# Kernel optimization log

Measured on AMD Instinct MI355X. Metric: run time of the kernel, lower is better.

## Reference

```python
import jax, jax.numpy as jnp
import numpy as np

B, Q, K, D, H = 8, 1024, 1024, 1024, 16
HD = D // H
FFN = 4 * D


def layer_norm(x, w, b, eps=1e-5):
    mu = jnp.mean(x, axis=-1, keepdims=True)
    var = jnp.var(x, axis=-1, keepdims=True)
    return (x - mu) * jax.lax.rsqrt(var + eps) * w + b


def setup_inputs() -> dict:
    key = jax.random.key(0)
    ks = jax.random.split(key, 10)
    query = jax.random.normal(ks[0], (B, Q, D), dtype=jnp.float32)
    key_value = jax.random.normal(ks[1], (B, K, D), dtype=jnp.float32)
    kpm = jax.random.randint(ks[2], (B, K), 0, 2).astype(bool)
    kpm = kpm.at[:, 0].set(True)  # guarantee >=1 valid key per row
    s = 0.02
    return {
        "query": query,
        "key_value": key_value,
        "key_padding_mask": kpm,
        "ln_q_w": jnp.ones((D,), jnp.float32), "ln_q_b": jnp.zeros((D,), jnp.float32),
        "ln_kv_w": jnp.ones((D,), jnp.float32), "ln_kv_b": jnp.zeros((D,), jnp.float32),
        "ln_f_w": jnp.ones((D,), jnp.float32), "ln_f_b": jnp.zeros((D,), jnp.float32),
        "in_proj_w": jax.random.normal(ks[3], (3 * D, D), jnp.float32) * s,
        "in_proj_b": jnp.zeros((3 * D,), jnp.float32),
        "out_proj_w": jax.random.normal(ks[4], (D, D), jnp.float32) * s,
        "out_proj_b": jnp.zeros((D,), jnp.float32),
        "ffn_w1": jax.random.normal(ks[5], (FFN, D), jnp.float32) * s,
        "ffn_b1": jnp.zeros((FFN,), jnp.float32),
        "ffn_w2": jax.random.normal(ks[6], (D, FFN), jnp.float32) * s,
        "ffn_b2": jnp.zeros((D,), jnp.float32),
    }


def reference(query, key_value, key_padding_mask,
              ln_q_w, ln_q_b, ln_kv_w, ln_kv_b, ln_f_w, ln_f_b,
              in_proj_w, in_proj_b, out_proj_w, out_proj_b,
              ffn_w1, ffn_b1, ffn_w2, ffn_b2):
    q_norm = layer_norm(query, ln_q_w, ln_q_b)
    kv_norm = layer_norm(key_value, ln_kv_w, ln_kv_b)

    Wq, Wk, Wv = jnp.split(in_proj_w, 3, axis=0)
    bq, bk, bv = jnp.split(in_proj_b, 3, axis=0)
    q = (q_norm @ Wq.T + bq).reshape(B, Q, H, HD).transpose(0, 2, 1, 3)  # (B,H,Q,hd)
    k = (kv_norm @ Wk.T + bk).reshape(B, K, H, HD).transpose(0, 2, 1, 3)
    v = (kv_norm @ Wv.T + bv).reshape(B, K, H, HD).transpose(0, 2, 1, 3)

    scale = 1.0 / jnp.sqrt(jnp.float32(HD))
    scores = jnp.einsum('bhqd,bhkd->bhqk', q * scale, k)  # (B,H,Q,K)
    scores = jnp.where(key_padding_mask[:, None, None, :], scores, -jnp.inf)
    attn = jax.nn.softmax(scores, axis=-1)

    attn_out = jnp.einsum('bhqk,bhkd->bhqd', attn, v)
    attn_out = attn_out.transpose(0, 2, 1, 3).reshape(B, Q, D)
    attn_out = attn_out @ out_proj_w.T + out_proj_b

    x = query + attn_out
    h = layer_norm(x, ln_f_w, ln_f_b)
    h = jax.nn.gelu(h @ ffn_w1.T + ffn_b1, approximate=False)
    x = x + (h @ ffn_w2.T + ffn_b2)

    attn_weights = jnp.mean(attn, axis=1)  # average over heads -> (B,Q,K)
    return x, attn_weights
```

## Files before the change

kernel.cpp:

```cpp
#include <hip/hip_runtime.h>
#include <math.h>

typedef short  s16x8 __attribute__((ext_vector_type(8)));
typedef short  s16x4 __attribute__((ext_vector_type(4)));
typedef float  f32x4 __attribute__((ext_vector_type(4)));

#define DEV static __device__ __forceinline__
#define M0SHIFT 3.0f
#define LOG2E   1.44269504088896f
#define SCL2F   0.18033688011112f

#if __has_builtin(__builtin_amdgcn_exp2f)
#define EXP2F(x) __builtin_amdgcn_exp2f(x)
#else
#define EXP2F(x) exp2f(x)
#endif

DEV float b2f(unsigned short h) {
    unsigned int u = ((unsigned int)h) << 16;
    float f; __builtin_memcpy(&f, &u, 4); return f;
}
DEV unsigned short f2b(float f) {
    unsigned int u; __builtin_memcpy(&u, &f, 4);
    unsigned int r = (u + 0x7fffu + ((u >> 16) & 1u)) >> 16;
    return (unsigned short)r;
}
DEV unsigned fb(float x) { unsigned u; __builtin_memcpy(&u, &x, 4); return u; }
DEV s16x4 pack4(float a0, float a1, float a2, float a3) {
    unsigned lo = __builtin_amdgcn_perm(fb(a1), fb(a0), 0x07060302u);
    unsigned hi = __builtin_amdgcn_perm(fb(a3), fb(a2), 0x07060302u);
    unsigned long long p = ((unsigned long long)hi << 32) | lo;
    s16x4 r; __builtin_memcpy(&r, &p, 8); return r;
}

#define GLD16(gp, lp) __builtin_amdgcn_global_load_lds( \
    (const __attribute__((address_space(1))) unsigned int*)(const void*)(gp), \
    (__attribute__((address_space(3))) unsigned int*)(void*)(lp), 16, 0, 0)

#if __has_builtin(__builtin_amdgcn_mfma_f32_16x16x16_bf16)
#define MFMA16(a, b, c) __builtin_amdgcn_mfma_f32_16x16x16_bf16(a, b, c, 0, 0, 0)
#else
#define MFMA16(a, b, c) __builtin_amdgcn_mfma_f32_16x16x16bf16_1k(a, b, c, 0, 0, 0)
#endif

DEV float ldsel(const void* p, size_t i, bool f32) {
    return f32 ? ((const float*)p)[i] : b2f(((const unsigned short*)p)[i]);
}
DEV s16x8 ld8sel(const void* p, size_t eidx, bool f32) {
    if (f32) {
        const float* f = (const float*)p + eidx;
        f32x4 a = *(const f32x4*)f;
        f32x4 b = *(const f32x4*)(f + 4);
        s16x8 o;
        o[0]=(short)f2b(a[0]); o[1]=(short)f2b(a[1]); o[2]=(short)f2b(a[2]); o[3]=(short)f2b(a[3]);
        o[4]=(short)f2b(b[0]); o[5]=(short)f2b(b[1]); o[6]=(short)f2b(b[2]); o[7]=(short)f2b(b[3]);
        return o;
    }
    return *(const s16x8*)((const unsigned short*)p + eidx);
}

__global__ __launch_bounds__(256) void dtype_probe(
    const unsigned int* __restrict__ q, int* __restrict__ flag)
{
    int t = threadIdx.x;
    int hits = 0;
    for (int i = t; i < 2048; i += 256) {
        unsigned e0 = (q[i] >> 7) & 0xFFu;
        hits += (e0 >= 0x70u && e0 <= 0x87u) ? 1 : 0;
    }
#pragma unroll
    for (int m = 32; m >= 1; m >>= 1) hits += __shfl_xor(hits, m);
    __shared__ int sh[4];
    if ((t & 63) == 0) sh[t >> 6] = hits;
    __syncthreads();
    if (t == 0) *flag = (sh[0] + sh[1] + sh[2] + sh[3] > 1024) ? 0 : 1;
}

__global__ __launch_bounds__(1024) void mask_prep(
    const unsigned int* __restrict__ w, const unsigned char* __restrict__ bytes,
    float* __restrict__ mf)
{
    __shared__ int flag;
    const int t = threadIdx.x;
    if (t == 0) flag = 0;
    __syncthreads();
    unsigned int a = w[t], b = w[t + 1024];
    if (a > 1u || b > 1u) flag = 1;
    __syncthreads();
    const int f = flag;
    const float NEGINF = -__builtin_inff();
#pragma unroll
    for (int i = 0; i < 8; i++) {
        int c = t * 8 + i;
        int v = f ? (int)(bytes[c] != 0) : (int)(w[c] != 0);
        mf[c] = v ? (-M0SHIFT * LOG2E) : NEGINF;
    }
}

struct CvtArgs { const void* s[8]; };
__global__ __launch_bounds__(256) void cvt_w(
    const int* __restrict__ flagp, CvtArgs a, unsigned short* __restrict__ dst)
{
    const int f = *flagp;
    size_t e = ((size_t)blockIdx.x * 256 + threadIdx.x) * 8;
    if (e >= 12592128u) return;
    const size_t off[9] = {0u, 3145728u, 4194304u, 8388608u, 12582912u,
                           12585984u, 12587008u, 12591104u, 12592128u};
    int s = 0;
    while (e >= off[s + 1]) s++;
    *(s16x8*)&dst[e] = ld8sel(a.s[s], e - off[s], f == 1);
}

__global__ __launch_bounds__(256) void ln_k(
    const int* __restrict__ flagp, int xmode, int wmode,
    const void* __restrict__ x1p, const void* __restrict__ w1p, const void* __restrict__ b1p,
    unsigned short* __restrict__ y1p,
    const void* __restrict__ x2p, const void* __restrict__ w2p, const void* __restrict__ b2p,
    unsigned short* __restrict__ y2p)
{
    const int f = *flagp;
    const bool xf = (xmode == 2) ? (f == 1) : (xmode == 1);
    const bool wf = (wmode == 2) ? (f == 1) : (wmode == 1);
    int row = blockIdx.x;
    const void* x = x1p; const void* wgt = w1p; const void* bias = b1p;
    unsigned short* y = y1p;
    if (x2p && row >= 8192) {
        row -= 8192; x = x2p; wgt = w2p; bias = b2p; y = y2p;
    }
    const int t = threadIdx.x;
    const int w = t >> 6, lane = t & 63;
    float f0, f1, f2, f3;
    if (xf) {
        f32x4 v = *(const f32x4*)((const float*)x + (size_t)row * 1024 + t * 4);
        f0 = v[0]; f1 = v[1]; f2 = v[2]; f3 = v[3];
    } else {
        s16x4 v = *(const s16x4*)((const unsigned short*)x + (size_t)row * 1024 + t * 4);
        f0 = b2f((unsigned short)v[0]); f1 = b2f((unsigned short)v[1]);
        f2 = b2f((unsigned short)v[2]); f3 = b2f((unsigned short)v[3]);
    }
    __shared__ float red[4];
    float s = f0 + f1 + f2 + f3;
#pragma unroll
    for (int m = 32; m >= 1; m >>= 1) s += __shfl_xor(s, m);
    if (lane == 0) red[w] = s;
    __syncthreads();
    float mu = (red[0] + red[1] + red[2] + red[3]) * (1.0f / 1024.0f);
    float d0 = f0 - mu, d1 = f1 - mu, d2 = f2 - mu, d3 = f3 - mu;
    float q = d0 * d0 + d1 * d1 + d2 * d2 + d3 * d3;
#pragma unroll
    for (int m = 32; m >= 1; m >>= 1) q += __shfl_xor(q, m);
    __syncthreads();
    if (lane == 0) red[w] = q;
    __syncthreads();
    float var = (red[0] + red[1] + red[2] + red[3]) * (1.0f / 1024.0f);
    float rs = rsqrtf(var + 1e-5f);
    s16x4 vo;
    vo[0] = (short)f2b(d0 * rs * ldsel(wgt, t*4+0, wf) + ldsel(bias, t*4+0, wf));
    vo[1] = (short)f2b(d1 * rs * ldsel(wgt, t*4+1, wf) + ldsel(bias, t*4+1, wf));
    vo[2] = (short)f2b(d2 * rs * ldsel(wgt, t*4+2, wf) + ldsel(bias, t*4+2, wf));
    vo[3] = (short)f2b(d3 * rs * ldsel(wgt, t*4+3, wf) + ldsel(bias, t*4+3, wf));
    *(s16x4*)&y[(size_t)row * 1024 + t * 4] = vo;
}

__global__ __launch_bounds__(256) void gemm_bt(
    const int* __restrict__ flagp,
    const unsigned short* __restrict__ A,
    const void* __restrict__ W, size_t woff, int wmode,
    const void* __restrict__ bias, size_t boff, int bmode,
    const void* __restrict__ res, int rmode,
    void* __restrict__ C, int omode,
    int M, int N, int Kd, int ldw, int ldc, int act)
{
    const int f = *flagp;
    const bool wf = (wmode == 2) && (f == 1);
    __shared__ alignas(16) unsigned short As[128 * 32];
    __shared__ alignas(16) unsigned short Bs[128 * 32];
    const int t = threadIdx.x;
    const int m0 = blockIdx.y * 128, n0 = blockIdx.x * 128;
    const int w = t >> 6, lane = t & 63, quad = lane >> 4, l16 = lane & 15;
    const int wm = (w >> 1) * 64, wn = (w & 1) * 64;
    const f32x4 zero = {0.f, 0.f, 0.f, 0.f};
    f32x4 acc[4][4];
#pragma unroll
    for (int i = 0; i < 4; i++)
#pragma unroll
        for (int j = 0; j < 4; j++) acc[i][j] = zero;
    const int r0 = t >> 2, c0 = (t & 3) * 8;
    unsigned short* AsW = As + (size_t)w * 512;
    unsigned short* BsW = Bs + (size_t)w * 512;
    const unsigned short* W16 = (const unsigned short*)W + woff;
    const float*          W32 = (const float*)W + woff;

    for (int kt = 0; kt < Kd; kt += 32) {
        GLD16(&A[(size_t)(m0 + r0) * Kd + kt + c0],      AsW);
        GLD16(&A[(size_t)(m0 + r0 + 64) * Kd + kt + c0], AsW + 2048);
        if (wf) {
            *(s16x8*)&Bs[r0 * 32 + c0]        = ld8sel(W32, (size_t)(n0 + r0) * ldw + kt + c0, true);
            *(s16x8*)&Bs[(r0 + 64) * 32 + c0] = ld8sel(W32, (size_t)(n0 + r0 + 64) * ldw + kt + c0, true);
        } else {
            GLD16(&W16[(size_t)(n0 + r0) * ldw + kt + c0],      BsW);
            GLD16(&W16[(size_t)(n0 + r0 + 64) * ldw + kt + c0], BsW + 2048);
        }
        __syncthreads();
        s16x8 af[4], bfr[4];
#pragma unroll
        for (int i = 0; i < 4; i++) {
            af[i]  = *(const s16x8*)&As[(wm + i * 16 + l16) * 32 + quad * 8];
            bfr[i] = *(const s16x8*)&Bs[(wn + i * 16 + l16) * 32 + quad * 8];
        }
#pragma unroll
        for (int mi = 0; mi < 4; mi++)
#pragma unroll
            for (int ni = 0; ni < 4; ni++)
                acc[mi][ni] = __builtin_amdgcn_mfma_f32_16x16x32_bf16(af[mi], bfr[ni], acc[mi][ni], 0, 0, 0);
        __syncthreads();
    }
    const bool bf = (bmode == 2) && (f == 1);
    const bool rf = (rmode == 2) || (rmode == 3 && f == 1);
    const bool of = (omode == 1) || (omode == 2 && f == 1);
#pragma unroll
    for (int mi = 0; mi < 4; mi++)
#pragma unroll
        for (int ni = 0; ni < 4; ni++)
#pragma unroll
            for (int r = 0; r < 4; r++) {
                int gr = m0 + wm + mi * 16 + quad * 4 + r;
                int gc = n0 + wn + ni * 16 + l16;
                float v = acc[mi][ni][r];
                if (bmode >= 0) v += ldsel(bias, boff + gc, bf);
                if (act) v = 0.5f * v * (1.f + erff(v * 0.70710678118f));
                if (rmode) v += ldsel(res, (size_t)gr * ldc + gc, rf);
                size_t ci = (size_t)gr * ldc + gc;
                if (of) ((float*)C)[ci] = v;
                else ((unsigned short*)C)[ci] = f2b(v);
            }
}

__global__ __launch_bounds__(512, 2) void gemm8(
    const unsigned short* __restrict__ A,
    const unsigned short* __restrict__ W, size_t woff,
    const unsigned short* __restrict__ bias, size_t boff,
    unsigned short* __restrict__ C,
    int Kd, int ldc, int act)
{
    __shared__ alignas(16) unsigned short lds[65536];
    const unsigned short* Wp = W + woff;
    const int t = threadIdx.x;
    const int w = t >> 6, lane = t & 63, quad = lane >> 4, l16 = lane & 15;
    const int wr = w >> 2, wcn = w & 3;

    const int gx = (int)gridDim.x;
    const int nwg = gx * (int)gridDim.y;
    const int lid = (int)blockIdx.y * gx + (int)blockIdx.x;
    const int swz = (lid & 7) * (nwg >> 3) + (lid >> 3);
    const int m0 = (swz / gx) * 256, n0 = (swz % gx) * 256;

    const int hrow = w * 16 + (lane >> 3);
    const int scol = ((lane & 7) ^ ((lane & 32) ? 2 : 0)) * 8;
    const int NT = Kd >> 6;

    const int swq = (l16 & 4) ? 16 : 0;
    const int ck0 = (quad * 8) ^ swq;
    const int ck1 = (32 + quad * 8) ^ swq;

    const f32x4 zero = {0.f, 0.f, 0.f, 0.f};
    f32x4 acc[8][4];
#pragma unroll
    for (int i = 0; i < 8; i++)
#pragma unroll
        for (int j = 0; j < 4; j++) acc[i][j] = zero;
    s16x8 aF[4][2], bLo[2][2], bHi[2][2];

#define SA8(bb,h,tt,g) GLD16(&A[(size_t)(m0 + (h)*128 + hrow + (g)*8) * Kd + (size_t)(tt)*64 + scol], \
                             &lds[(bb)*32768 + (h)*8192 + (w*16 + (g)*8)*64])
#define SB8(bb,h,tt,g) GLD16(&Wp[(size_t)(n0 + (h)*128 + hrow + (g)*8) * Kd + (size_t)(tt)*64 + scol], \
                             &lds[(bb)*32768 + 16384 + (h)*8192 + (w*16 + (g)*8)*64])
#define LDA8(bb,q) { _Pragma("unroll") for (int i_ = 0; i_ < 4; i_++) { \
        const int ar_ = (q)*128 + wr*64 + i_*16 + l16; \
        aF[i_][0] = *(const s16x8*)&lds[(bb)*32768 + ar_*64 + ck0]; \
        aF[i_][1] = *(const s16x8*)&lds[(bb)*32768 + ar_*64 + ck1]; } }
#define LDB8(bb,dst,q) { _Pragma("unroll") for (int j_ = 0; j_ < 2; j_++) { \
        const int br_ = (q)*128 + wcn*32 + j_*16 + l16; \
        dst[j_][0] = *(const s16x8*)&lds[(bb)*32768 + 16384 + br_*64 + ck0]; \
        dst[j_][1] = *(const s16x8*)&lds[(bb)*32768 + 16384 + br_*64 + ck1]; } }
#define MM8(mq,nq,bsrc) { __builtin_amdgcn_s_setprio(1); \
        _Pragma("unroll") for (int i_ = 0; i_ < 4; i_++) \
        _Pragma("unroll") for (int j_ = 0; j_ < 2; j_++) { \
            acc[(mq)*4+i_][(nq)*2+j_] = __builtin_amdgcn_mfma_f32_16x16x32_bf16(aF[i_][0], bsrc[j_][0], acc[(mq)*4+i_][(nq)*2+j_], 0, 0, 0); \
            acc[(mq)*4+i_][(nq)*2+j_] = __builtin_amdgcn_mfma_f32_16x16x32_bf16(aF[i_][1], bsrc[j_][1], acc[(mq)*4+i_][(nq)*2+j_], 0, 0, 0); } \
        __builtin_amdgcn_s_setprio(0); }
#define BAR8() __builtin_amdgcn_s_barrier()
#define VMW8(n) asm volatile("s_waitcnt vmcnt(" #n ")" ::: "memory")

    SA8(0, 0, 0, 0); SA8(0, 0, 0, 1);
    SB8(0, 0, 0, 0); SB8(0, 0, 0, 1);
    SB8(0, 1, 0, 0); SB8(0, 1, 0, 1);
    SA8(0, 1, 0, 0); SA8(0, 1, 0, 1);
    VMW8(4); BAR8();

    for (int tt = 0; tt < NT - 1; tt++) {
        const int bb = tt & 1, nb = bb ^ 1;
        SA8(nb, 0, tt + 1, 0); SA8(nb, 0, tt + 1, 1);
        LDA8(bb, 0); LDB8(bb, bLo, 0);
        MM8(0, 0, bLo);
        VMW8(4); BAR8();
        SB8(nb, 0, tt + 1, 0); SB8(nb, 0, tt + 1, 1);
        LDB8(bb, bHi, 1);
        MM8(0, 1, bHi);
        VMW8(4); BAR8();
        SB8(nb, 1, tt + 1, 0); SB8(nb, 1, tt + 1, 1);
        LDA8(bb, 1);
        MM8(1, 1, bHi);
        BAR8();
        SA8(nb, 1, tt + 1, 0); SA8(nb, 1, tt + 1, 1);
        MM8(1, 0, bLo);
        VMW8(4); BAR8();
    }
    {
        const int bb = (NT - 1) & 1;
        LDA8(bb, 0); LDB8(bb, bLo, 0); MM8(0, 0, bLo); VMW8(2); BAR8();
        LDB8(bb, bHi, 1);              MM8(0, 1, bHi); VMW8(0); BAR8();
        LDA8(bb, 1);                   MM8(1, 1, bHi);
        MM8(1, 0, bLo);
    }

#pragma unroll
    for (int nq = 0; nq < 2; nq++)
#pragma unroll
    for (int j = 0; j < 2; j++) {
        const int gc = n0 + nq * 128 + wcn * 32 + j * 16 + l16;
        const float bv = b2f(bias[boff + gc]);
#pragma unroll
        for (int mq = 0; mq < 2; mq++)
#pragma unroll
        for (int i = 0; i < 4; i++)
#pragma unroll
        for (int r = 0; r < 4; r++) {
            const int gr = m0 + mq * 128 + wr * 64 + i * 16 + quad * 4 + r;
            float v = acc[mq * 4 + i][nq * 2 + j][r] + bv;
            if (act) v = 0.5f * v * (1.f + erff(v * 0.70710678118f));
            C[(size_t)gr * ldc + gc] = f2b(v);
        }
    }
#undef SA8
#undef SB8
#undef LDA8
#undef LDB8
#undef MM8
#undef BAR8
#undef VMW8
}

__global__ __launch_bounds__(256) void repack_kv(
    const unsigned short* __restrict__ kvp,
    unsigned short* __restrict__ kf, unsigned short* __restrict__ vf)
{
    const bool isv = blockIdx.x >= 4096;
    int t = (blockIdx.x - (isv ? 4096 : 0)) * 256 + threadIdx.x;
    int lane = t & 63;
    int quad = lane >> 4, l16 = lane & 15;
    if (!isv) {
        int half = (t >> 6) & 1, tile = (t >> 7) & 63;
        int h = (t >> 13) & 15, b = t >> 17;
        s16x8 v = *(const s16x8*)&kvp[(size_t)(b * 1024 + tile * 16 + l16) * 2048
                                      + h * 64 + half * 32 + quad * 8];
        *(s16x8*)&kf[(size_t)t * 8] = v;
    } else {
        int dt = (t >> 6) & 3, kt5 = (t >> 8) & 31;
        int h = (t >> 13) & 15, b = t >> 17;
        int d = dt * 16 + l16;
        s16x8 o;
#pragma unroll
        for (int j = 0; j < 8; j++) {
            int k = kt5 * 32 + ((j < 4) ? (quad * 4 + j) : (16 + quad * 4 + j - 4));
            o[j] = (short)kvp[(size_t)(b * 1024 + k) * 2048 + 1024 + h * 64 + d];
        }
        *(s16x8*)&vf[(size_t)t * 8] = o;
    }
}

__global__ __launch_bounds__(256, 4) void flash_attn(
    const unsigned short* __restrict__ qp, const unsigned short* __restrict__ kf,
    const unsigned short* __restrict__ vf, const float* __restrict__ maskf,
    unsigned short* __restrict__ ao, float* __restrict__ ml)
{
    const int bh = blockIdx.x;
    const int b = bh >> 4, h = bh & 15;
    const int t = threadIdx.x, w = t >> 6, lane = t & 63, quad = lane >> 4, l16 = lane & 15;
    const int q0 = (blockIdx.y * 4 + w) * 32;
    const f32x4 zero = {0.f, 0.f, 0.f, 0.f};

    const unsigned short* kfb = kf + (size_t)bh * 65536;
    const unsigned short* vfb = vf + (size_t)bh * 65536;

    const size_t qbA = (size_t)(b * 1024 + q0 + l16) * 1024 + h * 64 + quad * 8;
    const size_t qbB = qbA + (size_t)16 * 1024;
    s16x8 qa0 = *(const s16x8*)&qp[qbA], qa1 = *(const s16x8*)&qp[qbA + 32];
    s16x8 qb0 = *(const s16x8*)&qp[qbB], qb1 = *(const s16x8*)&qp[qbB + 32];

    f32x4 OA[4], OB[4];
#pragma unroll
    for (int dt = 0; dt < 4; dt++) { OA[dt] = zero; OB[dt] = zero; }
    float lsA = 0.f, lsB = 0.f;

    for (int kt = 0; kt < 1024; kt += 32) {
        const int tile2 = (kt >> 4) * 2;
        s16x8 k00 = *(const s16x8*)&kfb[(size_t)(tile2 + 0) * 512 + lane * 8];
        s16x8 k01 = *(const s16x8*)&kfb[(size_t)(tile2 + 1) * 512 + lane * 8];
        s16x8 k10 = *(const s16x8*)&kfb[(size_t)(tile2 + 2) * 512 + lane * 8];
        s16x8 k11 = *(const s16x8*)&kfb[(size_t)(tile2 + 3) * 512 + lane * 8];
        const size_t vrow = (size_t)(kt >> 5) * 4;
        s16x8 vv[4];
#pragma unroll
        for (int dt = 0; dt < 4; dt++)
            vv[dt] = *(const s16x8*)&vfb[(vrow + dt) * 512 + lane * 8];

        f32x4 SA0 = __builtin_amdgcn_mfma_f32_16x16x32_bf16(k00, qa0, zero, 0, 0, 0);
        SA0 = __builtin_amdgcn_mfma_f32_16x16x32_bf16(k01, qa1, SA0, 0, 0, 0);
        f32x4 SA1 = __builtin_amdgcn_mfma_f32_16x16x32_bf16(k10, qa0, zero, 0, 0, 0);
        SA1 = __builtin_amdgcn_mfma_f32_16x16x32_bf16(k11, qa1, SA1, 0, 0, 0);
        f32x4 SB0 = __builtin_amdgcn_mfma_f32_16x16x32_bf16(k00, qb0, zero, 0, 0, 0);
        SB0 = __builtin_amdgcn_mfma_f32_16x16x32_bf16(k01, qb1, SB0, 0, 0, 0);
        f32x4 SB1 = __builtin_amdgcn_mfma_f32_16x16x32_bf16(k10, qb0, zero, 0, 0, 0);
        SB1 = __builtin_amdgcn_mfma_f32_16x16x32_bf16(k11, qb1, SB1, 0, 0, 0);

        f32x4 mk0 = *(const f32x4*)&maskf[b * 1024 + kt + quad * 4];
        f32x4 mk1 = *(const f32x4*)&maskf[b * 1024 + kt + 16 + quad * 4];
        float xA0[4], xA1[4], xB0[4], xB1[4];
#pragma unroll
        for (int r = 0; r < 4; r++) {
            xA0[r] = EXP2F(SA0[r] * SCL2F + mk0[r]);
            xA1[r] = EXP2F(SA1[r] * SCL2F + mk1[r]);
            xB0[r] = EXP2F(SB0[r] * SCL2F + mk0[r]);
            xB1[r] = EXP2F(SB1[r] * SCL2F + mk1[r]);
        }
        float rsA = (xA0[0] + xA0[1]) + (xA0[2] + xA0[3])
                  + (xA1[0] + xA1[1]) + (xA1[2] + xA1[3]);
        float rsB = (xB0[0] + xB0[1]) + (xB0[2] + xB0[3])
                  + (xB1[0] + xB1[1]) + (xB1[2] + xB1[3]);
        rsA += __shfl_xor(rsA, 16);  rsA += __shfl_xor(rsA, 32);
        rsB += __shfl_xor(rsB, 16);  rsB += __shfl_xor(rsB, 32);
        lsA += rsA;  lsB += rsB;

        s16x4 pA0 = pack4(xA0[0], xA0[1], xA0[2], xA0[3]);
        s16x4 pA1 = pack4(xA1[0], xA1[1], xA1[2], xA1[3]);
        s16x4 pB0 = pack4(xB0[0], xB0[1], xB0[2], xB0[3]);
        s16x4 pB1 = pack4(xB1[0], xB1[1], xB1[2], xB1[3]);
#pragma unroll
        for (int dt = 0; dt < 4; dt++) {
            s16x4 v0 = {vv[dt][0], vv[dt][1], vv[dt][2], vv[dt][3]};
            s16x4 v1 = {vv[dt][4], vv[dt][5], vv[dt][6], vv[dt][7]};
            OA[dt] = MFMA16(pA0, v0, OA[dt]);
            OA[dt] = MFMA16(pA1, v1, OA[dt]);
            OB[dt] = MFMA16(pB0, v0, OB[dt]);
            OB[dt] = MFMA16(pB1, v1, OB[dt]);
        }
    }
    float liA = (lsA > 0.f) ? 1.f / lsA : 0.f;
    float liB = (lsB > 0.f) ? 1.f / lsB : 0.f;
    float libA[4], libB[4];
#pragma unroll
    for (int r = 0; r < 4; r++) {
        libA[r] = __shfl(liA, quad * 4 + r);
        libB[r] = __shfl(liB, quad * 4 + r);
    }
#pragma unroll
    for (int dt = 0; dt < 4; dt++)
#pragma unroll
        for (int r = 0; r < 4; r++) {
            int qrA = q0 + quad * 4 + r;
            ao[(size_t)(b * 1024 + qrA) * 1024 + h * 64 + dt * 16 + l16] = f2b(OA[dt][r] * libA[r]);
            ao[(size_t)(b * 1024 + qrA + 16) * 1024 + h * 64 + dt * 16 + l16] = f2b(OB[dt][r] * libB[r]);
        }
    if (lane < 16) {
        size_t ix = ((size_t)(b * 16 + h) * 1024 + q0 + l16) * 2;
        ml[ix] = M0SHIFT;      ml[ix + 1] = lsA;
        ml[ix + 32] = M0SHIFT; ml[ix + 33] = lsB;
    }
}

__global__ __launch_bounds__(256) void attn_mean_k(
    const int* __restrict__ flagp,
    const unsigned short* __restrict__ qp, const unsigned short* __restrict__ kf,
    const float* __restrict__ maskf, const float* __restrict__ ml,
    void* __restrict__ dout)
{
    const bool of = (*flagp == 1);
    const size_t SHIFT = (size_t)8 * 1024 * 1024;
    const int b = blockIdx.x, q0 = blockIdx.y * 16;
    const int t = threadIdx.x, w = t >> 6, lane = t & 63, quad = lane >> 4, l16 = lane & 15;
    const int kbase = w * 256;
    const f32x4 zero = {0.f, 0.f, 0.f, 0.f};
    f32x4 acc[16];
#pragma unroll
    for (int i = 0; i < 16; i++) acc[i] = zero;
    float mka[16];
#pragma unroll
    for (int i = 0; i < 16; i++)
        mka[i] = maskf[b * 1024 + kbase + i * 16 + l16];
    for (int h = 0; h < 16; h++) {
        const size_t qb = (size_t)(b * 1024 + q0 + l16) * 1024 + h * 64 + quad * 8;
        s16x8 a0 = *(const s16x8*)&qp[qb];
        s16x8 a1 = *(const s16x8*)&qp[qb + 32];
        float cexp[4], lirow[4];
#pragma unroll
        for (int r = 0; r < 4; r++) {
            size_t ix = ((size_t)(b * 16 + h) * 1024 + q0 + quad * 4 + r) * 2;
            float lv = ml[ix + 1];
            cexp[r] = (M0SHIFT - ml[ix]) * LOG2E;
            lirow[r] = (lv > 0.f) ? 1.f / lv : 0.f;
        }
        const unsigned short* kfb = kf + ((size_t)(b * 16 + h) * 128 + (kbase >> 4) * 2) * 512;
#pragma unroll
        for (int i = 0; i < 16; i++) {
            s16x8 b0 = *(const s16x8*)&kfb[(size_t)(i * 2 + 0) * 512 + lane * 8];
            s16x8 b1 = *(const s16x8*)&kfb[(size_t)(i * 2 + 1) * 512 + lane * 8];
            f32x4 S = __builtin_amdgcn_mfma_f32_16x16x32_bf16(a0, b0, zero, 0, 0, 0);
            S = __builtin_amdgcn_mfma_f32_16x16x32_bf16(a1, b1, S, 0, 0, 0);
#pragma unroll
            for (int r = 0; r < 4; r++)
                acc[i][r] += EXP2F(S[r] * SCL2F + mka[i] + cexp[r]) * lirow[r];
        }
    }
#pragma unroll
    for (int i = 0; i < 16; i++)
#pragma unroll
        for (int r = 0; r < 4; r++) {
            int qrow = q0 + quad * 4 + r;
            size_t oi = SHIFT + (size_t)(b * 1024 + qrow) * 1024 + kbase + i * 16 + l16;
            float v = acc[i][r] * 0.0625f;
            if (of) ((float*)dout)[oi] = v;
            else ((unsigned short*)dout)[oi] = f2b(v);
        }
}

extern "C" void kernel_launch(void* const* d_in, const int* in_sizes, int n_in,
                              void* d_out, int out_size, void* d_ws, size_t ws_size,
                              hipStream_t stream) {
    const void* query = d_in[0];
    const void* keyv  = d_in[1];
    const void* maskr = d_in[2];
    const void* lqw = d_in[3];  const void* lqb = d_in[4];
    const void* lkw = d_in[5];  const void* lkb = d_in[6];
    const void* lfw = d_in[7];  const void* lfb = d_in[8];
    const void* ipw = d_in[9];  const void* ipb = d_in[10];
    const void* opw = d_in[11]; const void* opb = d_in[12];
    const void* w1  = d_in[13]; const void* b1  = d_in[14];
    const void* w2  = d_in[15]; const void* b2  = d_in[16];

    char* ws = (char*)d_ws;
    const size_t MB = 1024 * 1024;
    unsigned short* qn  = (unsigned short*)(ws + 0 * MB);
    unsigned short* kvn = (unsigned short*)(ws + 16 * MB);
    unsigned short* qpj = (unsigned short*)(ws + 32 * MB);
    unsigned short* kvp = (unsigned short*)(ws + 48 * MB);
    unsigned short* kfr = (unsigned short*)(ws + 80 * MB);
    unsigned short* vfr = (unsigned short*)(ws + 16 * MB);
    float*          ml  = (float*)(ws + 96 * MB);
    int*            fl  = (int*)(ws + 97 * MB);
    float*          mf  = (float*)(ws + 97 * MB + 256 * 1024);
    unsigned short* aco = (unsigned short*)(ws + 0 * MB);
    float*          xbf = (float*)(ws + 16 * MB);
    unsigned short* hn  = (unsigned short*)(ws + 48 * MB);
    unsigned short* g   = (unsigned short*)(ws + 64 * MB);
    unsigned short* wc  = (unsigned short*)(ws + 98 * MB);

    const bool big = ws_size >= (size_t)125 * MB;
    const size_t cWq = 0, cWk = 1048576, cWo = 3145728;
    const size_t cW1 = 4194304, cW2 = 8388608;
    const size_t cBq = 12582912, cBo = 12585984, cB1 = 12587008, cB2 = 12591104;

    const void *Wq, *Wk, *Wo, *Wf1, *Wf2, *Bq, *Bo, *Bf1, *Bf2;
    size_t wq_o, wk_o, wo_o, w1_o, w2_o, bq_o, bk_o, bo_o, b1_o, b2_o;
    int wm, bm;
    if (big) {
        Wq = Wk = Wo = Wf1 = Wf2 = Bq = Bo = Bf1 = Bf2 = wc;
        wq_o = cWq; wk_o = cWk; wo_o = cWo; w1_o = cW1; w2_o = cW2;
        bq_o = cBq; bk_o = cBq + 1024; bo_o = cBo; b1_o = cB1; b2_o = cB2;
        wm = 0; bm = 0;
    } else {
        Wq = Wk = ipw; Wo = opw; Wf1 = w1; Wf2 = w2;
        Bq = ipb; Bo = opb; Bf1 = b1; Bf2 = b2;
        wq_o = 0; wk_o = 1048576; wo_o = 0; w1_o = 0; w2_o = 0;
        bq_o = 0; bk_o = 1024; bo_o = 0; b1_o = 0; b2_o = 0;
        wm = 2; bm = 2;
    }

    dtype_probe<<<1, 256, 0, stream>>>((const unsigned int*)query, fl);
    mask_prep<<<1, 1024, 0, stream>>>((const unsigned int*)maskr, (const unsigned char*)maskr, mf);
    if (big) {
        CvtArgs ca; ca.s[0] = ipw; ca.s[1] = opw; ca.s[2] = w1; ca.s[3] = w2;
        ca.s[4] = ipb; ca.s[5] = opb; ca.s[6] = b1; ca.s[7] = b2;
        cvt_w<<<6149, 256, 0, stream>>>(fl, ca, wc);
    }

    ln_k<<<16384, 256, 0, stream>>>(fl, 2, 2, query, lqw, lqb, qn, keyv, lkw, lkb, kvn);

    gemm_bt<<<dim3(8, 64), 256, 0, stream>>>(fl, qn,  Wq, wq_o, wm, Bq, bq_o, bm,
                                             nullptr, 0, qpj, 0, 8192, 1024, 1024, 1024, 1024, 0);
    if (big) {
        gemm8<<<dim3(8, 32), 512, 0, stream>>>(kvn, wc, wk_o, wc, bk_o,
                                               kvp, 1024, 2048, 0);
    } else {
        gemm_bt<<<dim3(16, 64), 256, 0, stream>>>(fl, kvn, Wk, wk_o, wm, Bq, bk_o, bm,
                                                  nullptr, 0, kvp, 0, 8192, 2048, 1024, 1024, 2048, 0);
    }

    repack_kv<<<8192, 256, 0, stream>>>(kvp, kfr, vfr);
    flash_attn<<<dim3(128, 8), 256, 0, stream>>>(qpj, kfr, vfr, mf, aco, ml);
    attn_mean_k<<<dim3(8, 64), 256, 0, stream>>>(fl, qpj, kfr, mf, ml, d_out);

    gemm_bt<<<dim3(8, 64), 256, 0, stream>>>(fl, aco, Wo, wo_o, wm, Bo, bo_o, bm,
                                             query, 3, xbf, 1, 8192, 1024, 1024, 1024, 1024, 0);
    ln_k<<<8192, 256, 0, stream>>>(fl, 1, 2, xbf, lfw, lfb, hn,
                                   nullptr, nullptr, nullptr, nullptr);

    if (big) {
        gemm8<<<dim3(8, 32), 512, 0, stream>>>(hn, wc, w1_o, wc, b1_o,
                                               g, 1024, 2048, 1);
    } else {
        gemm_bt<<<dim3(16, 64), 256, 0, stream>>>(fl, hn, Wf1, w1_o, wm, Bf1, b1_o, bm,
                                                  nullptr, 0, g, 0, 8192, 2048, 1024, 1024, 2048, 1);
    }
    gemm_bt<<<dim3(8, 64), 256, 0, stream>>>(fl, g, Wf2, w2_o, wm, Bf2, b2_o, bm,
                                             xbf, 2, xbf, 1, 8192, 1024, 2048, 4096, 1024, 0);
    if (big) {
        gemm8<<<dim3(8, 32), 512, 0, stream>>>(hn, wc, w1_o + (size_t)2048 * 1024, wc, b1_o + 2048,
                                               g, 1024, 2048, 1);
    } else {
        gemm_bt<<<dim3(16, 64), 256, 0, stream>>>(fl, hn, Wf1, w1_o + (size_t)2048 * 1024, wm,
                                                  Bf1, b1_o + 2048, bm,
                                                  nullptr, 0, g, 0, 8192, 2048, 1024, 1024, 2048, 1);
    }
    gemm_bt<<<dim3(8, 64), 256, 0, stream>>>(fl, g, Wf2, w2_o + 2048, wm,
                                             nullptr, 0, -1,
                                             xbf, 2, d_out, 2, 8192, 1024, 2048, 4096, 1024, 0);
}
```

Measured before the change: 779.3 us.

## Add double-buffered 256x128 MFMA GEMM kernel for N=1024 projections

Adds gemm8n, a 512-thread GEMM with 256x128 tiles, double-buffered LDS loaded through direct global-to-LDS copies, swizzled LDS reads and 16x16x32 bf16 MFMAs, with bias and residual handling in the epilogue. On the converted-weight path it replaces the generic gemm_bt for the Q projection, the output projection and both FFN down-projection halves. The aim is better data reuse and load/compute overlap for the N=1024 GEMMs. The cost is higher LDS and register use per block, which may limit occupancy. The new calls rely on weight offsets (cWq, cWo, cW2 and matching bias offsets) that must be defined elsewhere in the file.

```diff
diff --git a/kernel.cpp b/kernel.cpp
--- a/kernel.cpp
+++ b/kernel.cpp
@@ -351,6 +351,115 @@
 #undef VMW8
 }
 
+__global__ __launch_bounds__(512, 2) void gemm8n(
+    const int* __restrict__ flagp,
+    const unsigned short* __restrict__ A,
+    const unsigned short* __restrict__ W, size_t woff, int ldw,
+    const unsigned short* __restrict__ bias, size_t boff, int bmode,
+    const void* __restrict__ res, int rmode,
+    void* __restrict__ C, int omode,
+    int Kd, int ldc)
+{
+    __shared__ alignas(16) unsigned short lds[49152];
+    const int f = *flagp;
+    const unsigned short* Wp = W + woff;
+    const int t = threadIdx.x;
+    const int w = t >> 6, lane = t & 63, quad = lane >> 4, l16 = lane & 15;
+    const int wr = w >> 2, wcn = w & 3;
+
+    const int gx = (int)gridDim.x;
+    const int nwg = gx * (int)gridDim.y;
+    const int lid = (int)blockIdx.y * gx + (int)blockIdx.x;
+    const int swz = (lid & 7) * (nwg >> 3) + (lid >> 3);
+    const int m0 = (swz / gx) * 256, n0 = (swz % gx) * 128;
+
+    const int hrow = w * 16 + (lane >> 3);
+    const int scol = ((lane & 7) ^ ((lane & 32) ? 2 : 0)) * 8;
+    const int NT = Kd >> 6;
+
+    const int swq = (l16 & 4) ? 16 : 0;
+    const int ck0 = (quad * 8) ^ swq;
+    const int ck1 = (32 + quad * 8) ^ swq;
+
+    const f32x4 zero = {0.f, 0.f, 0.f, 0.f};
+    f32x4 acc[8][2];
+#pragma unroll
+    for (int i = 0; i < 8; i++) { acc[i][0] = zero; acc[i][1] = zero; }
+    s16x8 aF[4][2], bF[2][2];
+
+#define SAN(bb,h,tt,g) GLD16(&A[(size_t)(m0 + (h)*128 + hrow + (g)*8) * Kd + (size_t)(tt)*64 + scol], \
+                             &lds[(bb)*24576 + (h)*8192 + (w*16 + (g)*8)*64])
+#define SBN(bb,tt,g)   GLD16(&Wp[(size_t)(n0 + hrow + (g)*8) * ldw + (size_t)(tt)*64 + scol], \
+                             &lds[(bb)*24576 + 16384 + (w*16 + (g)*8)*64])
+#define LDAN(bb,q) { _Pragma("unroll") for (int i_ = 0; i_ < 4; i_++) { \
+        const int ar_ = wr*64 + i_*16 + l16; \
+        aF[i_][0] = *(const s16x8*)&lds[(bb)*24576 + (q)*8192 + ar_*64 + ck0]; \
+        aF[i_][1] = *(const s16x8*)&lds[(bb)*24576 + (q)*8192 + ar_*64 + ck1]; } }
+#define LDBN(bb) { _Pragma("unroll") for (int j_ = 0; j_ < 2; j_++) { \
+        const int br_ = wcn*32 + j_*16 + l16; \
+        bF[j_][0] = *(const s16x8*)&lds[(bb)*24576 + 16384 + br_*64 + ck0]; \
+        bF[j_][1] = *(const s16x8*)&lds[(bb)*24576 + 16384 + br_*64 + ck1]; } }
+#define MMN(mq) { __builtin_amdgcn_s_setprio(1); \
+        _Pragma("unroll") for (int i_ = 0; i_ < 4; i_++) \
+        _Pragma("unroll") for (int j_ = 0; j_ < 2; j_++) { \
+            acc[(mq)*4+i_][j_] = __builtin_amdgcn_mfma_f32_16x16x32_bf16(aF[i_][0], bF[j_][0], acc[(mq)*4+i_][j_], 0, 0, 0); \
+            acc[(mq)*4+i_][j_] = __builtin_amdgcn_mfma_f32_16x16x32_bf16(aF[i_][1], bF[j_][1], acc[(mq)*4+i_][j_], 0, 0, 0); } \
+        __builtin_amdgcn_s_setprio(0); }
+#define BARN() __builtin_amdgcn_s_barrier()
+#define VMWN(n) asm volatile("s_waitcnt vmcnt(" #n ")" ::: "memory")
+
+    SAN(0, 0, 0, 0); SAN(0, 0, 0, 1);
+    SBN(0, 0, 0);    SBN(0, 0, 1);
+    SAN(0, 1, 0, 0); SAN(0, 1, 0, 1);
+    VMWN(2); BARN();
+
+    for (int tt = 0; tt < NT - 1; tt++) {
+        const int bb = tt & 1, nb = bb ^ 1;
+        SAN(nb, 0, tt + 1, 0); SAN(nb, 0, tt + 1, 1);
+        SBN(nb, tt + 1, 0);    SBN(nb, tt + 1, 1);
+        LDAN(bb, 0); LDBN(bb);
+        MMN(0);
+        VMWN(4); BARN();
+        SAN(nb, 1, tt + 1, 0); SAN(nb, 1, tt + 1, 1);
+        LDAN(bb, 1);
+        MMN(1);
+        VMWN(2); BARN();
+    }
+    {
+        const int bb = (NT - 1) & 1;
+        LDAN(bb, 0); LDBN(bb); MMN(0); VMWN(0); BARN();
+        LDAN(bb, 1);           MMN(1);
+    }
+
+    const bool rf = (rmode == 2) || (rmode == 3 && f == 1);
+    const bool of = (omode == 1) || (omode == 2 && f == 1);
+#pragma unroll
+    for (int j = 0; j < 2; j++) {
+        const int gc = n0 + wcn * 32 + j * 16 + l16;
+        const float bv = (bmode >= 0) ? b2f(bias[boff + gc]) : 0.f;
+#pragma unroll
+        for (int mq = 0; mq < 2; mq++)
+#pragma unroll
+        for (int i = 0; i < 4; i++)
+#pragma unroll
+        for (int r = 0; r < 4; r++) {
+            const int gr = m0 + mq * 128 + wr * 64 + i * 16 + quad * 4 + r;
+            float v = acc[mq * 4 + i][j][r] + bv;
+            if (rmode) v += ldsel(res, (size_t)gr * ldc + gc, rf);
+            size_t ci = (size_t)gr * ldc + gc;
+            if (of) ((float*)C)[ci] = v;
+            else ((unsigned short*)C)[ci] = f2b(v);
+        }
+    }
+#undef SAN
+#undef SBN
+#undef LDAN
+#undef LDBN
+#undef MMN
+#undef BARN
+#undef VMWN
+}
+
 __global__ __launch_bounds__(256) void repack_kv(
     const unsigned short* __restrict__ kvp,
     unsigned short* __restrict__ kf, unsigned short* __restrict__ vf)
@@ -596,12 +705,14 @@
 
     ln_k<<<16384, 256, 0, stream>>>(fl, 2, 2, query, lqw, lqb, qn, keyv, lkw, lkb, kvn);
 
-    gemm_bt<<<dim3(8, 64), 256, 0, stream>>>(fl, qn,  Wq, wq_o, wm, Bq, bq_o, bm,
-                                             nullptr, 0, qpj, 0, 8192, 1024, 1024, 1024, 1024, 0);
     if (big) {
+        gemm8n<<<dim3(8, 32), 512, 0, stream>>>(fl, qn, wc, cWq, 1024, wc, cBq, 0,
+                                                nullptr, 0, qpj, 0, 1024, 1024);
         gemm8<<<dim3(8, 32), 512, 0, stream>>>(kvn, wc, wk_o, wc, bk_o,
                                                kvp, 1024, 2048, 0);
     } else {
+        gemm_bt<<<dim3(8, 64), 256, 0, stream>>>(fl, qn,  Wq, wq_o, wm, Bq, bq_o, bm,
+                                                 nullptr, 0, qpj, 0, 8192, 1024, 1024, 1024, 1024, 0);
         gemm_bt<<<dim3(16, 64), 256, 0, stream>>>(fl, kvn, Wk, wk_o, wm, Bq, bk_o, bm,
                                                   nullptr, 0, kvp, 0, 8192, 2048, 1024, 1024, 2048, 0);
     }
@@ -610,29 +721,35 @@
     flash_attn<<<dim3(128, 8), 256, 0, stream>>>(qpj, kfr, vfr, mf, aco, ml);
     attn_mean_k<<<dim3(8, 64), 256, 0, stream>>>(fl, qpj, kfr, mf, ml, d_out);
 
-    gemm_bt<<<dim3(8, 64), 256, 0, stream>>>(fl, aco, Wo, wo_o, wm, Bo, bo_o, bm,
-                                             query, 3, xbf, 1, 8192, 1024, 1024, 1024, 1024, 0);
+    if (big) {
+        gemm8n<<<dim3(8, 32), 512, 0, stream>>>(fl, aco, wc, cWo, 1024, wc, cBo, 0,
+                                                query, 3, xbf, 1, 1024, 1024);
+    } else {
+        gemm_bt<<<dim3(8, 64), 256, 0, stream>>>(fl, aco, Wo, wo_o, wm, Bo, bo_o, bm,
+                                                 query, 3, xbf, 1, 8192, 1024, 1024, 1024, 1024, 0);
+    }
     ln_k<<<8192, 256, 0, stream>>>(fl, 1, 2, xbf, lfw, lfb, hn,
                                    nullptr, nullptr, nullptr, nullptr);
 
     if (big) {
         gemm8<<<dim3(8, 32), 512, 0, stream>>>(hn, wc, w1_o, wc, b1_o,
                                                g, 1024, 2048, 1);
+        gemm8n<<<dim3(8, 32), 512, 0, stream>>>(fl, g, wc, cW2, 4096, wc, cB2, 0,
+                                                xbf, 2, xbf, 1, 2048, 1024);
+        gemm8<<<dim3(8, 32), 512, 0, stream>>>(hn, wc, w1_o + (size_t)2048 * 1024, wc, b1_o + 2048,
+                                               g, 1024, 2048, 1);
+        gemm8n<<<dim3(8, 32), 512, 0, stream>>>(fl, g, wc, cW2 + 2048, 4096, nullptr, 0, -1,
+                                                xbf, 2, d_out, 2, 2048, 1024);
     } else {
         gemm_bt<<<dim3(16, 64), 256, 0, stream>>>(fl, hn, Wf1, w1_o, wm, Bf1, b1_o, bm,
                                                   nullptr, 0, g, 0, 8192, 2048, 1024, 1024, 2048, 1);
-    }
-    gemm_bt<<<dim3(8, 64), 256, 0, stream>>>(fl, g, Wf2, w2_o, wm, Bf2, b2_o, bm,
-                                             xbf, 2, xbf, 1, 8192, 1024, 2048, 4096, 1024, 0);
-    if (big) {
-        gemm8<<<dim3(8, 32), 512, 0, stream>>>(hn, wc, w1_o + (size_t)2048 * 1024, wc, b1_o + 2048,
-                                               g, 1024, 2048, 1);
-    } else {
+        gemm_bt<<<dim3(8, 64), 256, 0, stream>>>(fl, g, Wf2, w2_o, wm, Bf2, b2_o, bm,
+                                                 xbf, 2, xbf, 1, 8192, 1024, 2048, 4096, 1024, 0);
         gemm_bt<<<dim3(16, 64), 256, 0, stream>>>(fl, hn, Wf1, w1_o + (size_t)2048 * 1024, wm,
                                                   Bf1, b1_o + 2048, bm,
                                                   nullptr, 0, g, 0, 8192, 2048, 1024, 1024, 2048, 1);
-    }
-    gemm_bt<<<dim3(8, 64), 256, 0, stream>>>(fl, g, Wf2, w2_o + 2048, wm,
-                                             nullptr, 0, -1,
-                                             xbf, 2, d_out, 2, 8192, 1024, 2048, 4096, 1024, 0);
-}
+        gemm_bt<<<dim3(8, 64), 256, 0, stream>>>(fl, g, Wf2, w2_o + 2048, wm,
+                                                 nullptr, 0, -1,
+                                                 xbf, 2, d_out, 2, 8192, 1024, 2048, 4096, 1024, 0);
+    }
+}
```

New measurement: 708.4 us. 9.1% less time.
